# Kernel tuning notes

Hardware: AMD Instinct MI355X
Metric: run time of the kernel (lower is better)

Reference implementation:

```python
import jax, jax.numpy as jnp
import numpy as np

B, S, HID = 2, 2048, 1024
NH = 16
HD = HID // NH  # 64
ROPE_BASE = 10000.0
NEG_INF = -1e9


def _rope_emb(seq_len):
    # emb = cat(sin, cos) over head_dim, shape [1, S, 1, HD]
    inv_freq = 1.0 / (ROPE_BASE ** (jnp.arange(0, HD, 2, dtype=jnp.float32) / HD))
    pos = jnp.arange(seq_len, dtype=jnp.float32)
    sincos = pos[:, None] * inv_freq[None, :]            # [S, HD/2]
    emb = jnp.concatenate([jnp.sin(sincos), jnp.cos(sincos)], axis=-1)  # [S, HD]
    return emb[None, :, None, :]


def _apply_rope(x, emb):
    # Faithful to the (quirky) torch code: cos = emb[..., 1::2], sin = emb[..., ::2]
    cos = emb[..., 1::2]
    sin = emb[..., ::2]
    xe = x[..., ::2]
    xo = x[..., 1::2]
    return jnp.concatenate([xe * cos - xo * sin, xe * sin + xo * cos], axis=-1)


def setup_inputs() -> dict:
    key = jax.random.key(0)
    ks = jax.random.split(key, 5)
    hidden_states = jax.random.normal(ks[0], (B, S, HID), dtype=jnp.float32)
    # causal additive mask, broadcast over batch/heads
    causal = jnp.tril(jnp.ones((S, S), dtype=bool))
    attention_mask = jnp.where(causal, 0.0, NEG_INF).astype(jnp.float32)[None, None]
    scale = 1.0 / np.sqrt(HID)
    w_q = jax.random.normal(ks[1], (HID, HID), dtype=jnp.float32) * scale
    w_k = jax.random.normal(ks[2], (HID, HID), dtype=jnp.float32) * scale
    w_v = jax.random.normal(ks[3], (HID, HID), dtype=jnp.float32) * scale
    w_o = jax.random.normal(ks[4], (HID, HID), dtype=jnp.float32) * scale
    return {"hidden_states": hidden_states, "attention_mask": attention_mask,
            "w_q": w_q, "w_k": w_k, "w_v": w_v, "w_o": w_o}


def reference(hidden_states, attention_mask, w_q, w_k, w_v, w_o):
    b, s, _ = hidden_states.shape
    # torch Linear: x @ W.T (W is [out, in])
    q = (hidden_states @ w_q.T).reshape(b, s, NH, HD)
    k = (hidden_states @ w_k.T).reshape(b, s, NH, HD)
    v = (hidden_states @ w_v.T).reshape(b, s, NH, HD)
    emb = _rope_emb(s)
    q = _apply_rope(q, emb)
    k = _apply_rope(k, emb)
    # [b, h, s, d]
    q = q.transpose(0, 2, 1, 3)
    k = k.transpose(0, 2, 1, 3)
    v = v.transpose(0, 2, 1, 3)
    scores = jnp.einsum('bhqd,bhkd->bhqk', q, k) / np.sqrt(HD)
    scores = scores + attention_mask
    attn = jax.nn.softmax(scores, axis=-1)
    out = jnp.einsum('bhqk,bhkd->bhqd', attn, v)
    out = out.transpose(0, 2, 1, 3).reshape(b, s, HID)
    return out @ w_o.T
```

## Files before the change

kernel.cpp:

```cpp
#include <hip/hip_runtime.h>
#include <hip/hip_bf16.h>
#include <math.h>

typedef unsigned short u16;
typedef unsigned int   u32;
typedef unsigned long long u64;
typedef __attribute__((ext_vector_type(8))) short bf16x8;
typedef __attribute__((ext_vector_type(4))) short bf16x4;
typedef __attribute__((ext_vector_type(4))) float f32x4;

#define B_   2
#define S_   2048
#define HID_ 1024
#define NH_  16
#define HD_  64
#define MR_  (B_*S_)

#define QSCALE 0.1803368801111137f

__device__ __forceinline__ u16 f2bf(float f) {
  union { float f; u32 u; } x; x.f = f;
  u32 r = x.u + 0x7fffu + ((x.u >> 16) & 1u);
  return (u16)(r >> 16);
}
__device__ __forceinline__ void gload16(const void* g, void* l) {
  __builtin_amdgcn_global_load_lds(
      (const __attribute__((address_space(1))) u32*)g,
      (__attribute__((address_space(3))) u32*)l, 16, 0, 0);
}

__global__ void k_cvt_all(const float* __restrict__ hs, const float* __restrict__ wq,
                          const float* __restrict__ wk, const float* __restrict__ wv,
                          const float* __restrict__ wo, ushort4* __restrict__ dst) {
  int i = blockIdx.x * blockDim.x + threadIdx.x;
  const float4* src;
  int idx;
  if (i < 1048576) {
    src = (const float4*)hs; idx = i;
  } else {
    int j = i - 1048576;
    int w = j >> 18; idx = j & 262143;
    src = (const float4*)(w == 0 ? wq : w == 1 ? wk : w == 2 ? wv : wo);
  }
  float4 v = src[idx];
  ushort4 o;
  o.x = f2bf(v.x); o.y = f2bf(v.y); o.z = f2bf(v.z); o.w = f2bf(v.w);
  dst[i] = o;
}

__global__ void k_rope_table(float2* __restrict__ tab) {
  int t = blockIdx.x * blockDim.x + threadIdx.x;
  int p = t >> 5, j = t & 31;
  double fp = (double)p;
  double c, s;
  if (j < 16) {
    s = sin(fp * pow(10000.0, -(2.0 * j) / 32.0));
    c = sin(fp * pow(10000.0, -(2.0 * j + 1.0) / 32.0));
  } else {
    s = cos(fp * pow(10000.0, -(2.0 * j - 32.0) / 32.0));
    c = cos(fp * pow(10000.0, -(2.0 * j - 31.0) / 32.0));
  }
  tab[p * 32 + j] = make_float2((float)c, (float)s);
}

template <int MODE, int BM>
__global__ __launch_bounds__(512) void k_gemm_bt(
    const u16* __restrict__ A,
    const u16* __restrict__ W0, const u16* __restrict__ W1, const u16* __restrict__ W2,
    u16* __restrict__ O0, u16* __restrict__ O1, u16* __restrict__ O2,
    float* __restrict__ OF, const float2* __restrict__ tab, int K) {
  constexpr int WR = BM / 4;
  constexpr int MI = BM / 64;
  __shared__ __align__(16) u16 Al[2][BM * 64];
  __shared__ __align__(16) u16 Bl[2][128 * 64];

  int tid = threadIdx.x;
  int lane = tid & 63, wave = tid >> 6;
  int m0 = blockIdx.y * BM;
  int nt0 = blockIdx.x * 128;
  int wi = nt0 >> 10;
  const u16* W = (wi == 0) ? W0 : (wi == 1 ? W1 : W2);
  int n0 = nt0 & 1023;
  int wm = wave >> 1, wn = wave & 1;
  int lg = lane >> 4, lr = lane & 15;

  f32x4 acc[MI][4];
  const f32x4 vz = {0.f, 0.f, 0.f, 0.f};
#pragma unroll
  for (int i = 0; i < MI; ++i)
#pragma unroll
    for (int j = 0; j < 4; ++j) acc[i][j] = vz;

  auto STAGE = [&](int t_, int bs_) {
    int k0 = t_ * 64;
#pragma unroll
    for (int it = 0; it < BM / 64; ++it) {
      int c = it * 512 + tid;
      int row = c >> 3;
      int cw = (c & 7) ^ (row & 7);
      gload16(&A[(size_t)(m0 + row) * K + k0 + cw * 8], &Al[bs_][(it * 512 + wave * 64) * 8]);
    }
#pragma unroll
    for (int it = 0; it < 2; ++it) {
      int c = it * 512 + tid;
      int row = c >> 3;
      int cw = (c & 7) ^ (row & 7);
      gload16(&W[(size_t)(n0 + row) * K + k0 + cw * 8], &Bl[bs_][(it * 512 + wave * 64) * 8]);
    }
  };

  int nkt = K >> 6;
  STAGE(0, 0);

  for (int t = 0; t < nkt; ++t) {
    int cur = t & 1;
    if (t + 1 < nkt) {
      STAGE(t + 1, cur ^ 1);
      if (MODE == 0) asm volatile("s_waitcnt vmcnt(4)" ::: "memory");
      else           asm volatile("s_waitcnt vmcnt(3)" ::: "memory");
    } else {
      asm volatile("s_waitcnt vmcnt(0)" ::: "memory");
    }
    __builtin_amdgcn_s_barrier();
    __builtin_amdgcn_sched_barrier(0);

#pragma unroll
    for (int kk = 0; kk < 2; ++kk) {
      bf16x8 af[MI], bfr[4];
#pragma unroll
      for (int mi = 0; mi < MI; ++mi) {
        int row = wm * WR + mi * 16 + lr;
        int ci = (kk * 4 + lg) ^ (row & 7);
        af[mi] = *(const bf16x8*)&Al[cur][row * 64 + ci * 8];
      }
#pragma unroll
      for (int ni = 0; ni < 4; ++ni) {
        int row = wn * 64 + ni * 16 + lr;
        int ci = (kk * 4 + lg) ^ (row & 7);
        bfr[ni] = *(const bf16x8*)&Bl[cur][row * 64 + ci * 8];
      }
      __builtin_amdgcn_s_setprio(1);
#pragma unroll
      for (int mi = 0; mi < MI; ++mi)
#pragma unroll
        for (int ni = 0; ni < 4; ++ni)
          acc[mi][ni] = __builtin_amdgcn_mfma_f32_16x16x32_bf16(af[mi], bfr[ni], acc[mi][ni], 0, 0, 0);
      __builtin_amdgcn_s_setprio(0);
    }
    __builtin_amdgcn_sched_barrier(0);
    __builtin_amdgcn_s_barrier();
  }

  if (MODE == 1) {
#pragma unroll
    for (int mi = 0; mi < MI; ++mi)
#pragma unroll
      for (int ni = 0; ni < 4; ++ni)
#pragma unroll
        for (int r = 0; r < 4; ++r) {
          int grow = m0 + wm * WR + mi * 16 + lg * 4 + r;
          int gcol = n0 + wn * 64 + ni * 16 + lr;
          OF[(size_t)grow * 1024 + gcol] = acc[mi][ni][r];
        }
    return;
  }

  if (wi == 2) {
#pragma unroll
    for (int mi = 0; mi < MI; ++mi) {
      int grow0 = m0 + wm * WR + mi * 16 + lg * 4;
      int bb = grow0 >> 11;
      int s = grow0 & 2047;
#pragma unroll
      for (int ni = 0; ni < 4; ++ni) {
        int gcol = n0 + wn * 64 + ni * 16 + lr;
        int h = gcol >> 6, dd = gcol & 63;
        u64 pk = (u64)f2bf(acc[mi][ni][0]) |
                 ((u64)f2bf(acc[mi][ni][1]) << 16) |
                 ((u64)f2bf(acc[mi][ni][2]) << 32) |
                 ((u64)f2bf(acc[mi][ni][3]) << 48);
        *(u64*)&O2[((size_t)(bb * NH_ + h) * HD_ + dd) * S_ + s] = pk;
      }
    }
  } else {
    u16* OB = wi ? O1 : O0;
    float sc = wi ? 1.0f : QSCALE;
#pragma unroll
    for (int mi = 0; mi < MI; ++mi) {
#pragma unroll
      for (int ni = 0; ni < 4; ++ni) {
        int gcol = n0 + wn * 64 + ni * 16 + lr;
        int h = gcol >> 6;
        int j = (gcol & 63) >> 1;
        bool even = !(gcol & 1);
        int ocol = h * 64 + (even ? j : 32 + j);
#pragma unroll
        for (int r = 0; r < 4; ++r) {
          float val = acc[mi][ni][r];
          float pv = __shfl_xor(val, 1);
          int grow = m0 + wm * WR + mi * 16 + lg * 4 + r;
          int s = grow & 2047;
          float2 cs = tab[s * 32 + j];
          float xe = even ? val : pv;
          float xo = even ? pv : val;
          float res = even ? (xe * cs.x - xo * cs.y) : (xe * cs.y + xo * cs.x);
          OB[(size_t)grow * 1024 + ocol] = f2bf(res * sc);
        }
      }
    }
  }
}

__global__ __launch_bounds__(256, 4) void k_attn(
    const u16* __restrict__ Q, const u16* __restrict__ Kr, const u16* __restrict__ VT,
    u16* __restrict__ O) {
  __shared__ __align__(16) u16 Kl[2][64 * 64];
  __shared__ __align__(16) u16 Vl[2][64 * 64];

  int tid = threadIdx.x, lane = tid & 63, wave = tid >> 6;
  int id = blockIdx.x;
  int qt = 31 - (id >> 5);
  int bh = id & 31;
  int b = bh >> 4, h = bh & 15;
  int lg = lane >> 4, lr = lane & 15;
  int bS = b * S_;
  int nkt = qt + 1;
  int q0 = qt * 64 + wave * 16;

  const u16* vtb = &VT[(size_t)bh * HD_ * S_];
  int l8 = lane >> 3, l7 = lane & 7;
  int sl = l7 ^ l8;

  auto STAGE = [&](int kt_, int bs_) {
#pragma unroll
    for (int it = 0; it < 2; ++it) {
      int rb = wave * 16 + it * 8;
      int r = rb + l8;
      gload16(&Kr[(size_t)(bS + kt_ * 64 + r) * HID_ + h * HD_ + sl * 8],
              &Kl[bs_][rb * 64]);
      gload16(&vtb[(size_t)r * S_ + kt_ * 64 + sl * 8],
              &Vl[bs_][rb * 64]);
    }
  };

  STAGE(0, 0);

  bf16x8 qf[2];
#pragma unroll
  for (int kk = 0; kk < 2; ++kk)
    qf[kk] = *(const bf16x8*)
        &Q[(size_t)(bS + q0 + lr) * HID_ + h * HD_ + kk * 32 + lg * 8];

  f32x4 acc[4];
  const f32x4 vz = {0.f, 0.f, 0.f, 0.f};
#pragma unroll
  for (int df = 0; df < 4; ++df) acc[df] = vz;
  float m_ = -1e30f;
  float l_ = 0.f;

  for (int kt = 0; kt < nkt; ++kt) {
    int cur = kt & 1;
    if (kt + 1 < nkt) {
      STAGE(kt + 1, cur ^ 1);
      asm volatile("s_waitcnt vmcnt(4)" ::: "memory");
    } else {
      asm volatile("s_waitcnt vmcnt(0)" ::: "memory");
    }
    __builtin_amdgcn_s_barrier();
    __builtin_amdgcn_sched_barrier(0);

    bf16x8 kfr[4][2];
#pragma unroll
    for (int kf = 0; kf < 4; ++kf) {
      int row = kf * 16 + lr;
#pragma unroll
      for (int kk = 0; kk < 2; ++kk) {
        int ci = (kk * 4 + lg) ^ (row & 7);
        kfr[kf][kk] = *(const bf16x8*)&Kl[cur][row * 64 + ci * 8];
      }
    }

    f32x4 st[4];
#pragma unroll
    for (int kf = 0; kf < 4; ++kf) st[kf] = vz;
    __builtin_amdgcn_s_setprio(1);
#pragma unroll
    for (int kk = 0; kk < 2; ++kk)
#pragma unroll
      for (int kf = 0; kf < 4; ++kf)
        st[kf] = __builtin_amdgcn_mfma_f32_16x16x32_bf16(
            kfr[kf][kk], qf[kk], st[kf], 0, 0, 0);
    __builtin_amdgcn_s_setprio(0);

    if (kt == qt) {
      int qg = q0 + lr;
#pragma unroll
      for (int kf = 0; kf < 4; ++kf)
#pragma unroll
        for (int r = 0; r < 4; ++r) {
          int kg = kt * 64 + kf * 16 + lg * 4 + r;
          if (kg > qg) st[kf][r] = -1e30f;
        }
    }

    float tmx = -1e30f;
#pragma unroll
    for (int kf = 0; kf < 4; ++kf)
#pragma unroll
      for (int r = 0; r < 4; ++r) tmx = fmaxf(tmx, st[kf][r]);
    tmx = fmaxf(tmx, __shfl_xor(tmx, 16));
    tmx = fmaxf(tmx, __shfl_xor(tmx, 32));

    if (!__all(tmx <= m_ + 8.f)) {
      float mn = fmaxf(m_, tmx);
      float rsc = __builtin_amdgcn_exp2f(m_ - mn);
      l_ *= rsc;
#pragma unroll
      for (int df = 0; df < 4; ++df) acc[df] *= rsc;
      m_ = mn;
    }
    float mb = m_;
    float ts = 0.f;
    bf16x4 pb[4];
#pragma unroll
    for (int kf = 0; kf < 4; ++kf) {
#pragma unroll
      for (int r = 0; r < 4; ++r) {
        float e = __builtin_amdgcn_exp2f(st[kf][r] - mb);
        st[kf][r] = e;
        ts += e;
      }
      u32 w0, w1;
      asm("v_cvt_pk_bf16_f32 %0, %1, %2" : "=v"(w0) : "v"(st[kf][0]), "v"(st[kf][1]));
      asm("v_cvt_pk_bf16_f32 %0, %1, %2" : "=v"(w1) : "v"(st[kf][2]), "v"(st[kf][3]));
      union { u32 u[2]; bf16x4 v; } pk;
      pk.u[0] = w0; pk.u[1] = w1;
      pb[kf] = pk.v;
    }
    ts += __shfl_xor(ts, 16);
    ts += __shfl_xor(ts, 32);
    l_ += ts;

    __builtin_amdgcn_s_setprio(1);
#pragma unroll
    for (int df = 0; df < 4; ++df) {
      int row = df * 16 + lr;
#pragma unroll
      for (int kf = 0; kf < 4; ++kf) {
        int slot = (kf * 2 + (lg >> 1)) ^ (row & 7);
        bf16x4 vfr = *(const bf16x4*)&Vl[cur][row * 64 + slot * 8 + (lg & 1) * 4];
        acc[df] = __builtin_amdgcn_mfma_f32_16x16x16bf16_1k(
            vfr, pb[kf], acc[df], 0, 0, 0);
      }
    }
    __builtin_amdgcn_s_setprio(0);

    __builtin_amdgcn_sched_barrier(0);
    __builtin_amdgcn_s_barrier();
  }

  float inv = 1.0f / l_;
  int grow = bS + q0 + lr;
#pragma unroll
  for (int df = 0; df < 4; ++df) {
    u64 pk = (u64)f2bf(acc[df][0] * inv) |
             ((u64)f2bf(acc[df][1] * inv) << 16) |
             ((u64)f2bf(acc[df][2] * inv) << 32) |
             ((u64)f2bf(acc[df][3] * inv) << 48);
    *(u64*)&O[(size_t)grow * HID_ + h * HD_ + df * 16 + lg * 4] = pk;
  }
}

extern "C" void kernel_launch(void* const* d_in, const int* in_sizes, int n_in,
                              void* d_out, int out_size, void* d_ws, size_t ws_size,
                              hipStream_t stream) {
  const float* hs = (const float*)d_in[0];
  const float* wq = (const float*)d_in[2];
  const float* wk = (const float*)d_in[3];
  const float* wv = (const float*)d_in[4];
  const float* wo = (const float*)d_in[5];
  float* out = (float*)d_out;

  char* ws = (char*)d_ws;
  const size_t P = (size_t)MR_ * HID_ * 2;
  u16* Xb  = (u16*)(ws);
  u16* Wqb = (u16*)(ws + P);
  u16* Wkb = (u16*)(ws + P + (size_t)HID_ * HID_ * 2);
  u16* Wvb = (u16*)(ws + P + (size_t)HID_ * HID_ * 4);
  u16* Wob = (u16*)(ws + P + (size_t)HID_ * HID_ * 6);
  u16* q_r = (u16*)(ws + 2 * P);
  u16* k_r = (u16*)(ws + 3 * P);
  u16* vt  = (u16*)(ws + 4 * P);
  float2* tab = (float2*)(ws + 5 * P);
  u16* attn_o = Xb;

  k_cvt_all<<<8192, 256, 0, stream>>>(hs, wq, wk, wv, wo, (ushort4*)ws);
  k_rope_table<<<256, 256, 0, stream>>>(tab);

  k_gemm_bt<0, 128><<<dim3(24, 32), 512, 0, stream>>>(
      Xb, Wqb, Wkb, Wvb, q_r, k_r, vt, nullptr, tab, HID_);

  k_attn<<<1024, 256, 0, stream>>>(q_r, k_r, vt, attn_o);

  k_gemm_bt<1, 64><<<dim3(8, 64), 512, 0, stream>>>(
      attn_o, Wob, Wob, Wob, nullptr, nullptr, nullptr, out, nullptr, HID_);
}
```

Baseline: 121.0 us.

## Process two 64-row query tiles per attention block to reuse K/V tiles

Each attention block now covers 128 query rows: every wave holds two 16-row query fragments, 64 rows apart, and runs the online softmax and PV update for both against the same staged K/V tile. The grid shrinks from 1024 to 512 blocks and the causal key-tile count becomes 2*qt+2. The aim is to halve global and LDS K/V traffic per query row and to reuse each K fragment across two MFMA chains. In exchange, register pressure rises and there are fewer blocks to balance causal work across CUs. The first fragment also does a fully masked extra key tile on the diagonal.

```diff
diff --git a/kernel.cpp b/kernel.cpp
--- a/kernel.cpp
+++ b/kernel.cpp
@@ -219,13 +219,13 @@
 
   int tid = threadIdx.x, lane = tid & 63, wave = tid >> 6;
   int id = blockIdx.x;
-  int qt = 31 - (id >> 5);
+  int qt = 15 - (id >> 5);
   int bh = id & 31;
   int b = bh >> 4, h = bh & 15;
   int lg = lane >> 4, lr = lane & 15;
   int bS = b * S_;
-  int nkt = qt + 1;
-  int q0 = qt * 64 + wave * 16;
+  int nkt = 2 * qt + 2;
+  int qb = qt * 128 + wave * 16;
 
   const u16* vtb = &VT[(size_t)bh * HD_ * S_];
   int l8 = lane >> 3, l7 = lane & 7;
@@ -245,18 +245,22 @@
 
   STAGE(0, 0);
 
-  bf16x8 qf[2];
-#pragma unroll
-  for (int kk = 0; kk < 2; ++kk)
-    qf[kk] = *(const bf16x8*)
-        &Q[(size_t)(bS + q0 + lr) * HID_ + h * HD_ + kk * 32 + lg * 8];
-
-  f32x4 acc[4];
+  bf16x8 qf[2][2];
+#pragma unroll
+  for (int f = 0; f < 2; ++f)
+#pragma unroll
+    for (int kk = 0; kk < 2; ++kk)
+      qf[f][kk] = *(const bf16x8*)
+          &Q[(size_t)(bS + qb + f * 64 + lr) * HID_ + h * HD_ + kk * 32 + lg * 8];
+
+  f32x4 acc[2][4];
   const f32x4 vz = {0.f, 0.f, 0.f, 0.f};
 #pragma unroll
-  for (int df = 0; df < 4; ++df) acc[df] = vz;
-  float m_ = -1e30f;
-  float l_ = 0.f;
+  for (int f = 0; f < 2; ++f)
+#pragma unroll
+    for (int df = 0; df < 4; ++df) acc[f][df] = vz;
+  float m_[2] = {-1e30f, -1e30f};
+  float l_[2] = {0.f, 0.f};
 
   for (int kt = 0; kt < nkt; ++kt) {
     int cur = kt & 1;
@@ -269,105 +273,107 @@
     __builtin_amdgcn_s_barrier();
     __builtin_amdgcn_sched_barrier(0);
 
-    bf16x8 kfr[4][2];
+    f32x4 st[2][4];
+#pragma unroll
+    for (int kf = 0; kf < 4; ++kf) { st[0][kf] = vz; st[1][kf] = vz; }
+    __builtin_amdgcn_s_setprio(1);
 #pragma unroll
     for (int kf = 0; kf < 4; ++kf) {
       int row = kf * 16 + lr;
-#pragma unroll
-      for (int kk = 0; kk < 2; ++kk) {
-        int ci = (kk * 4 + lg) ^ (row & 7);
-        kfr[kf][kk] = *(const bf16x8*)&Kl[cur][row * 64 + ci * 8];
-      }
-    }
-
-    f32x4 st[4];
-#pragma unroll
-    for (int kf = 0; kf < 4; ++kf) st[kf] = vz;
-    __builtin_amdgcn_s_setprio(1);
-#pragma unroll
-    for (int kk = 0; kk < 2; ++kk)
+      int ci0 = lg ^ (row & 7);
+      int ci1 = (4 + lg) ^ (row & 7);
+      bf16x8 k0 = *(const bf16x8*)&Kl[cur][row * 64 + ci0 * 8];
+      bf16x8 k1 = *(const bf16x8*)&Kl[cur][row * 64 + ci1 * 8];
+      st[0][kf] = __builtin_amdgcn_mfma_f32_16x16x32_bf16(k0, qf[0][0], st[0][kf], 0, 0, 0);
+      st[0][kf] = __builtin_amdgcn_mfma_f32_16x16x32_bf16(k1, qf[0][1], st[0][kf], 0, 0, 0);
+      st[1][kf] = __builtin_amdgcn_mfma_f32_16x16x32_bf16(k0, qf[1][0], st[1][kf], 0, 0, 0);
+      st[1][kf] = __builtin_amdgcn_mfma_f32_16x16x32_bf16(k1, qf[1][1], st[1][kf], 0, 0, 0);
+    }
+    __builtin_amdgcn_s_setprio(0);
+
+#pragma unroll
+    for (int f = 0; f < 2; ++f) {
+      int ktm = 2 * qt + f;
+      if (kt >= ktm) {
+        int qg = qb + f * 64 + lr;
+#pragma unroll
+        for (int kf = 0; kf < 4; ++kf)
+#pragma unroll
+          for (int r = 0; r < 4; ++r) {
+            int kg = kt * 64 + kf * 16 + lg * 4 + r;
+            if (kg > qg) st[f][kf][r] = -1e30f;
+          }
+      }
+
+      float tmx = -1e30f;
 #pragma unroll
       for (int kf = 0; kf < 4; ++kf)
-        st[kf] = __builtin_amdgcn_mfma_f32_16x16x32_bf16(
-            kfr[kf][kk], qf[kk], st[kf], 0, 0, 0);
-    __builtin_amdgcn_s_setprio(0);
-
-    if (kt == qt) {
-      int qg = q0 + lr;
-#pragma unroll
-      for (int kf = 0; kf < 4; ++kf)
+#pragma unroll
+        for (int r = 0; r < 4; ++r) tmx = fmaxf(tmx, st[f][kf][r]);
+      tmx = fmaxf(tmx, __shfl_xor(tmx, 16));
+      tmx = fmaxf(tmx, __shfl_xor(tmx, 32));
+
+      if (!__all(tmx <= m_[f] + 8.f)) {
+        float mn = fmaxf(m_[f], tmx);
+        float rsc = __builtin_amdgcn_exp2f(m_[f] - mn);
+        l_[f] *= rsc;
+#pragma unroll
+        for (int df = 0; df < 4; ++df) acc[f][df] *= rsc;
+        m_[f] = mn;
+      }
+      float mb = m_[f];
+      float ts = 0.f;
+      bf16x4 pb[4];
+#pragma unroll
+      for (int kf = 0; kf < 4; ++kf) {
 #pragma unroll
         for (int r = 0; r < 4; ++r) {
-          int kg = kt * 64 + kf * 16 + lg * 4 + r;
-          if (kg > qg) st[kf][r] = -1e30f;
+          float e = __builtin_amdgcn_exp2f(st[f][kf][r] - mb);
+          st[f][kf][r] = e;
+          ts += e;
         }
-    }
-
-    float tmx = -1e30f;
-#pragma unroll
-    for (int kf = 0; kf < 4; ++kf)
-#pragma unroll
-      for (int r = 0; r < 4; ++r) tmx = fmaxf(tmx, st[kf][r]);
-    tmx = fmaxf(tmx, __shfl_xor(tmx, 16));
-    tmx = fmaxf(tmx, __shfl_xor(tmx, 32));
-
-    if (!__all(tmx <= m_ + 8.f)) {
-      float mn = fmaxf(m_, tmx);
-      float rsc = __builtin_amdgcn_exp2f(m_ - mn);
-      l_ *= rsc;
-#pragma unroll
-      for (int df = 0; df < 4; ++df) acc[df] *= rsc;
-      m_ = mn;
-    }
-    float mb = m_;
-    float ts = 0.f;
-    bf16x4 pb[4];
-#pragma unroll
-    for (int kf = 0; kf < 4; ++kf) {
-#pragma unroll
-      for (int r = 0; r < 4; ++r) {
-        float e = __builtin_amdgcn_exp2f(st[kf][r] - mb);
-        st[kf][r] = e;
-        ts += e;
-      }
-      u32 w0, w1;
-      asm("v_cvt_pk_bf16_f32 %0, %1, %2" : "=v"(w0) : "v"(st[kf][0]), "v"(st[kf][1]));
-      asm("v_cvt_pk_bf16_f32 %0, %1, %2" : "=v"(w1) : "v"(st[kf][2]), "v"(st[kf][3]));
-      union { u32 u[2]; bf16x4 v; } pk;
-      pk.u[0] = w0; pk.u[1] = w1;
-      pb[kf] = pk.v;
-    }
-    ts += __shfl_xor(ts, 16);
-    ts += __shfl_xor(ts, 32);
-    l_ += ts;
-
-    __builtin_amdgcn_s_setprio(1);
-#pragma unroll
-    for (int df = 0; df < 4; ++df) {
-      int row = df * 16 + lr;
-#pragma unroll
-      for (int kf = 0; kf < 4; ++kf) {
-        int slot = (kf * 2 + (lg >> 1)) ^ (row & 7);
-        bf16x4 vfr = *(const bf16x4*)&Vl[cur][row * 64 + slot * 8 + (lg & 1) * 4];
-        acc[df] = __builtin_amdgcn_mfma_f32_16x16x16bf16_1k(
-            vfr, pb[kf], acc[df], 0, 0, 0);
-      }
-    }
-    __builtin_amdgcn_s_setprio(0);
+        u32 w0, w1;
+        asm("v_cvt_pk_bf16_f32 %0, %1, %2" : "=v"(w0) : "v"(st[f][kf][0]), "v"(st[f][kf][1]));
+        asm("v_cvt_pk_bf16_f32 %0, %1, %2" : "=v"(w1) : "v"(st[f][kf][2]), "v"(st[f][kf][3]));
+        union { u32 u[2]; bf16x4 v; } pk;
+        pk.u[0] = w0; pk.u[1] = w1;
+        pb[kf] = pk.v;
+      }
+      ts += __shfl_xor(ts, 16);
+      ts += __shfl_xor(ts, 32);
+      l_[f] += ts;
+
+      __builtin_amdgcn_s_setprio(1);
+#pragma unroll
+      for (int df = 0; df < 4; ++df) {
+        int row = df * 16 + lr;
+#pragma unroll
+        for (int kf = 0; kf < 4; ++kf) {
+          int slot = (kf * 2 + (lg >> 1)) ^ (row & 7);
+          bf16x4 vfr = *(const bf16x4*)&Vl[cur][row * 64 + slot * 8 + (lg & 1) * 4];
+          acc[f][df] = __builtin_amdgcn_mfma_f32_16x16x16bf16_1k(
+              vfr, pb[kf], acc[f][df], 0, 0, 0);
+        }
+      }
+      __builtin_amdgcn_s_setprio(0);
+    }
 
     __builtin_amdgcn_sched_barrier(0);
     __builtin_amdgcn_s_barrier();
   }
 
-  float inv = 1.0f / l_;
-  int grow = bS + q0 + lr;
-#pragma unroll
-  for (int df = 0; df < 4; ++df) {
-    u64 pk = (u64)f2bf(acc[df][0] * inv) |
-             ((u64)f2bf(acc[df][1] * inv) << 16) |
-             ((u64)f2bf(acc[df][2] * inv) << 32) |
-             ((u64)f2bf(acc[df][3] * inv) << 48);
-    *(u64*)&O[(size_t)grow * HID_ + h * HD_ + df * 16 + lg * 4] = pk;
+#pragma unroll
+  for (int f = 0; f < 2; ++f) {
+    float inv = 1.0f / l_[f];
+    int grow = bS + qb + f * 64 + lr;
+#pragma unroll
+    for (int df = 0; df < 4; ++df) {
+      u64 pk = (u64)f2bf(acc[f][df][0] * inv) |
+               ((u64)f2bf(acc[f][df][1] * inv) << 16) |
+               ((u64)f2bf(acc[f][df][2] * inv) << 32) |
+               ((u64)f2bf(acc[f][df][3] * inv) << 48);
+      *(u64*)&O[(size_t)grow * HID_ + h * HD_ + df * 16 + lg * 4] = pk;
+    }
   }
 }
 
@@ -400,7 +406,7 @@
   k_gemm_bt<0, 128><<<dim3(24, 32), 512, 0, stream>>>(
       Xb, Wqb, Wkb, Wvb, q_r, k_r, vt, nullptr, tab, HID_);
 
-  k_attn<<<1024, 256, 0, stream>>>(q_r, k_r, vt, attn_o);
+  k_attn<<<512, 256, 0, stream>>>(q_r, k_r, vt, attn_o);
 
   k_gemm_bt<1, 64><<<dim3(8, 64), 512, 0, stream>>>(
       attn_o, Wob, Wob, Wob, nullptr, nullptr, nullptr, out, nullptr, HID_);
```

After: 163.6 us. 1.35x slower.
